# Kernel tuning notes

Hardware: AMD Instinct MI355X
Metric: run time of the kernel (lower is better)

The kernel has to match this reference:

```python
import jax, jax.numpy as jnp
import numpy as np

T, B, I, H, O = 512, 64, 256, 512, 256


def _lstm(x_proj, h0, c0, W_hh, dtype=jnp.float32):
    """Run an LSTM over precomputed input projections.
    x_proj: (T, B, 4H) = x @ W_ih.T + b_ih (+ b_hh folded in).
    PyTorch gate order: i, f, g, o.
    Returns (hs: (T,B,H), h_final: (B,H))."""
    def step(carry, xp_t):
        h, c = carry
        gates = xp_t + h @ W_hh.T  # (B, 4H)
        i, f, g, o = jnp.split(gates, 4, axis=-1)
        c = jax.nn.sigmoid(f) * c + jax.nn.sigmoid(i) * jnp.tanh(g)
        h = jax.nn.sigmoid(o) * jnp.tanh(c)
        return (h, c), h
    (hT, cT), hs = jax.lax.scan(step, (h0, c0), x_proj)
    return hs, hT


def setup_inputs() -> dict:
    key = jax.random.key(0)
    ks = jax.random.split(key, 16)
    s1 = 1.0 / np.sqrt(H)
    u = lambda k, shape: jax.random.uniform(k, shape, jnp.float32, -s1, s1)
    inputs = jax.random.normal(ks[0], (T, B, I), jnp.float32)
    return {
        "inputs": inputs,
        # LSTM1 (input I -> hidden H), PyTorch layout: W_ih (4H, I), W_hh (4H, H)
        "W_ih1": u(ks[1], (4 * H, I)), "W_hh1": u(ks[2], (4 * H, H)),
        "b_ih1": u(ks[3], (4 * H,)), "b_hh1": u(ks[4], (4 * H,)),
        # LSTM2 (hidden H -> hidden H)
        "W_ih2": u(ks[5], (4 * H, H)), "W_hh2": u(ks[6], (4 * H, H)),
        "b_ih2": u(ks[7], (4 * H,)), "b_hh2": u(ks[8], (4 * H,)),
        # Linear H -> O
        "W_lin": u(ks[9], (O, H)), "b_lin": u(ks[10], (O,)),
        # fixed initial hidden/cell states (module buffers in the original)
        "h1_0": jax.random.normal(ks[11], (B, H), jnp.float32),
        "c1_0": jax.random.uniform(ks[12], (B, H), jnp.float32),
        "h2_0": jax.random.normal(ks[13], (B, H), jnp.float32),
        "c2_0": jax.random.normal(ks[14], (B, H), jnp.float32),
    }


def reference(inputs, W_ih1, W_hh1, b_ih1, b_hh1, W_ih2, W_hh2, b_ih2, b_hh2,
              W_lin, b_lin, h1_0, c1_0, h2_0, c2_0):
    # Encoder: precompute input projections for all timesteps at once.
    xp1 = jnp.einsum('tbi,gi->tbg', inputs, W_ih1) + b_ih1 + b_hh1  # (T,B,4H)
    _, h1T = _lstm(xp1, h1_0, c1_0, W_hh1)
    # Decoder input = final encoder hidden repeated T times -> constant projection.
    xp2_one = h1T @ W_ih2.T + b_ih2 + b_hh2  # (B,4H)
    xp2 = jnp.broadcast_to(xp2_one, (T, B, 4 * H))
    out2, _ = _lstm(xp2, h2_0, c2_0, W_hh2)  # (T,B,H)
    out_lin = jnp.einsum('tbh,oh->tbo', out2, W_lin) + b_lin
    return out_lin.reshape(-1, O)  # (T*B, O)
```

## Files before the change

kernel.cpp:

```cpp
#include <hip/hip_runtime.h>
#include <hip/hip_bf16.h>

#define T_ 512
#define B_ 64
#define I_ 256
#define H_ 512
#define O_ 256
#define NGB 32
#define NLB 8
#define NBLK (NGB + NLB)
#define NTHR 512
#define NTOT (NBLK * NTHR)

typedef unsigned short u16;
typedef unsigned int u32;
typedef unsigned long long u64;
typedef short bf16x8 __attribute__((ext_vector_type(8)));
typedef float f32x4 __attribute__((ext_vector_type(4)));
typedef u32 u32x4 __attribute__((ext_vector_type(4)));

#define CT_LIN   0
#define CT_B0    64

#define WS_XBF   4096
#define WS_WHH1  (WS_XBF   + 16777216)
#define WS_WIH1  (WS_WHH1  + 2097152)
#define WS_WIH2  (WS_WIH1  + 1048576)
#define WS_WHH2  (WS_WIH2  + 2097152)
#define WS_WLIN  (WS_WHH2  + 2097152)
#define WS_B1    (WS_WLIN  + 262144)
#define WS_B2    (WS_B1    + 8192)
#define WS_H1T   (WS_B2    + 8192)
#define WS_H2T   (WS_H1T   + 262144)
#define WS_END   (WS_H2T   + 524288)

__device__ __forceinline__ u16 f2bf(float f) {
  union { float f; unsigned u; } v; v.f = f;
  unsigned r = v.u + 0x7FFFu + ((v.u >> 16) & 1u);
  return (u16)(r >> 16);
}
__device__ __forceinline__ float sigm(float x)  { return 1.0f / (1.0f + __expf(-x)); }
__device__ __forceinline__ float tanh_(float x) { return 1.0f - 2.0f / (__expf(2.0f * x) + 1.0f); }
__device__ __forceinline__ bf16x8 ldg8(const u16* p) { return *(const bf16x8*)p; }
__device__ __forceinline__ void ast32(u32* p, u32 v) {
  __hip_atomic_store(p, v, __ATOMIC_RELAXED, __HIP_MEMORY_SCOPE_AGENT);
}
#define MFMA16(a, b, c) __builtin_amdgcn_mfma_f32_16x16x32_bf16((a), (b), (c), 0, 0, 0)

__device__ __forceinline__ void cvt8(const float* s, u16* dst) {
  bf16x8 v;
  #pragma unroll
  for (int jj = 0; jj < 8; jj++) v[jj] = (short)f2bf(s[jj]);
  *(bf16x8*)dst = v;
}

template<bool LINCHK, int SLP>
__device__ __forceinline__ void pollTile(const u32* pbw, u32 tag,
                                         const u32* lfp, int ltgt, u32* pk) {
  while (1) {
    u32 w[16];
    bool ok = true;
    u32x4 A, B2, C2, D2;
    if (LINCHK) {
      u32 lv;
      asm volatile(
        "global_load_dwordx4 %0, %5, off sc0 sc1\n\t"
        "global_load_dwordx4 %1, %5, off offset:16 sc0 sc1\n\t"
        "global_load_dwordx4 %2, %5, off offset:32 sc0 sc1\n\t"
        "global_load_dwordx4 %3, %5, off offset:48 sc0 sc1\n\t"
        "global_load_dword   %4, %6, off sc0 sc1\n\t"
        "s_waitcnt vmcnt(0)"
        : "=&v"(A), "=&v"(B2), "=&v"(C2), "=&v"(D2), "=&v"(lv)
        : "v"(pbw), "v"(lfp)
        : "memory");
      ok = (int)lv >= ltgt;
    } else {
      asm volatile(
        "global_load_dwordx4 %0, %4, off sc0 sc1\n\t"
        "global_load_dwordx4 %1, %4, off offset:16 sc0 sc1\n\t"
        "global_load_dwordx4 %2, %4, off offset:32 sc0 sc1\n\t"
        "global_load_dwordx4 %3, %4, off offset:48 sc0 sc1\n\t"
        "s_waitcnt vmcnt(0)"
        : "=&v"(A), "=&v"(B2), "=&v"(C2), "=&v"(D2)
        : "v"(pbw)
        : "memory");
    }
    #pragma unroll
    for (int m = 0; m < 4; m++) {
      w[m] = A[m]; w[4 + m] = B2[m]; w[8 + m] = C2[m]; w[12 + m] = D2[m];
    }
    #pragma unroll
    for (int m = 0; m < 16; m++) ok = ok && ((w[m] >> 16) == tag);
    if (__all(ok)) {
      #pragma unroll
      for (int m = 0; m < 8; m++)
        pk[m] = (w[2 * m] & 0xFFFFu) | (w[2 * m + 1] << 16);
      return;
    }
    if (SLP) __builtin_amdgcn_s_sleep(SLP);
  }
}

__device__ __forceinline__ void gbar0(u32* cnt, unsigned target) {
  __syncthreads();
  if (threadIdx.x == 0) {
    __threadfence();
    __hip_atomic_fetch_add(cnt, 1u, __ATOMIC_RELAXED, __HIP_MEMORY_SCOPE_AGENT);
    while (__hip_atomic_load(cnt, __ATOMIC_RELAXED, __HIP_MEMORY_SCOPE_AGENT) < target)
      __builtin_amdgcn_s_sleep(2);
    __threadfence();
  }
  __syncthreads();
}

__global__ void init_cnt(char* ws) {
  for (int i = threadIdx.x; i < 1024; i += 256)
    __hip_atomic_store((u32*)ws + i, 0u, __ATOMIC_RELAXED, __HIP_MEMORY_SCOPE_AGENT);
}

__global__ void __launch_bounds__(NTHR, 1) lstm_ae_kernel(
    const float* __restrict__ xin,
    const float* __restrict__ Wih1, const float* __restrict__ Whh1,
    const float* __restrict__ bih1, const float* __restrict__ bhh1,
    const float* __restrict__ Wih2, const float* __restrict__ Whh2,
    const float* __restrict__ bih2, const float* __restrict__ bhh2,
    const float* __restrict__ Wlin, const float* __restrict__ blin,
    const float* __restrict__ h10, const float* __restrict__ c10,
    const float* __restrict__ h20, const float* __restrict__ c20,
    float* __restrict__ out, char* __restrict__ ws) {
  char* ctrl = ws;
  u32* linf  = (u32*)(ctrl + CT_LIN);
  u16* xbf   = (u16*)(ws + WS_XBF);
  u16* whh1f = (u16*)(ws + WS_WHH1);
  u16* wih1f = (u16*)(ws + WS_WIH1);
  u16* wih2f = (u16*)(ws + WS_WIH2);
  u16* whh2f = (u16*)(ws + WS_WHH2);
  u16* wlinf = (u16*)(ws + WS_WLIN);
  float* b1  = (float*)(ws + WS_B1);
  float* b2  = (float*)(ws + WS_B2);
  u32* h1s   = (u32*)(ws + WS_H1T);
  u32* h2s   = (u32*)(ws + WS_H2T);

  __shared__ __align__(16) u16 Ald[16 * 512];
  __shared__ float exch[4 * 16 * 68];

  const int tid = blockIdx.x * NTHR + threadIdx.x;

  for (int c = tid; c < T_ * B_ * I_ / 8; c += NTOT)
    cvt8(xin + c * 8, xbf + c * 8);
  for (int c = tid; c < (1 << 17); c += NTOT) {
    int lane = c & 63, kt = (c >> 6) & 15, g = (c >> 10) & 3, n = c >> 12;
    int row = g * 512 + n * 16 + (lane & 15);
    int k   = kt * 32 + (lane >> 4) * 8;
    cvt8(Whh1 + row * 512 + k, whh1f + c * 8);
  }
  for (int c = tid; c < (1 << 16); c += NTOT) {
    int lane = c & 63, kt = (c >> 6) & 7, g = (c >> 9) & 3, n = c >> 11;
    int row = g * 512 + n * 16 + (lane & 15);
    int k   = kt * 32 + (lane >> 4) * 8;
    cvt8(Wih1 + row * 256 + k, wih1f + c * 8);
  }
  for (int c = tid; c < (1 << 17); c += NTOT) {
    int lane = c & 63, kt = (c >> 6) & 15, g = (c >> 10) & 3, n = c >> 12;
    int row = g * 512 + n * 16 + (lane & 15);
    int k   = kt * 32 + (lane >> 4) * 8;
    cvt8(Wih2 + row * 512 + k, wih2f + c * 8);
    cvt8(Whh2 + row * 512 + k, whh2f + c * 8);
  }
  for (int c = tid; c < (1 << 14); c += NTOT) {
    int lane = c & 63, kt = (c >> 6) & 15, nt = (c >> 10) & 1, l = c >> 11;
    int row = l * 32 + nt * 16 + (lane & 15);
    int k   = kt * 32 + (lane >> 4) * 8;
    cvt8(Wlin + row * 512 + k, wlinf + c * 8);
  }
  for (int i2 = tid; i2 < 2048; i2 += NTOT) {
    b1[i2] = bih1[i2] + bhh1[i2];
    b2[i2] = bih2[i2] + bhh2[i2];
  }
  for (int c = tid; c < (1 << 16); c += NTOT) {
    int slot = c >> 15, rem = c & 32767;
    int mtd = rem >> 13, r2 = rem & 8191, row = r2 >> 9, col = r2 & 511;
    u32 v = 0xFFFF0000u;
    if (slot == 0) v = (u32)f2bf(h10[(mtd * 16 + row) * 512 + col]);
    h1s[c] = v;
  }
  for (int c = tid; c < (1 << 17); c += NTOT) {
    int slot = c >> 15, rem = c & 32767;
    int mtd = rem >> 13, r2 = rem & 8191, row = r2 >> 9, col = r2 & 511;
    u32 v = 0xFFFF0000u;
    if (slot == 0) v = (u32)f2bf(h20[(mtd * 16 + row) * 512 + col]);
    h2s[c] = v;
  }

  gbar0((u32*)(ctrl + CT_B0), NBLK);

  const int lane = threadIdx.x & 63;
  const int w    = threadIdx.x >> 6;
  const int l15  = lane & 15;
  const int l31  = lane & 31;
  const int qd   = lane >> 4;
  const int prow = 2 * w + (lane >> 5);
  const int swz  = (prow & 7) << 4;
  const int pb32 = prow * 512 + l31 * 16;

  #define AFRAG(ktv) (*(const bf16x8*)((const char*)Ald + l15 * 1024 + \
                       (((ktv) * 64 + qd * 16) ^ ((l15 & 7) << 4))))
  #define STAGEA(pk) do { \
      u32x4 v0_ = {(pk)[0], (pk)[1], (pk)[2], (pk)[3]}; \
      u32x4 v1_ = {(pk)[4], (pk)[5], (pk)[6], (pk)[7]}; \
      char* ab_ = (char*)Ald + prow * 1024; \
      *(u32x4*)(ab_ + ((l31 * 32 +  0) ^ swz)) = v0_; \
      *(u32x4*)(ab_ + ((l31 * 32 + 16) ^ swz)) = v1_; \
    } while (0)

  if (blockIdx.x < NGB) {
    const int mt = blockIdx.x >> 3;
    const int j  = blockIdx.x & 7;
    const int g  = w >> 1;
    const int half = w & 1;
    const int nt0 = j * 4 + half * 2;

    bf16x8 Wr0[16], Wr1[16];
    #pragma unroll
    for (int kt = 0; kt < 16; kt++) {
      Wr0[kt] = ldg8(whh1f + ((size_t)((nt0 + 0) * 4 + g) * 16 + kt) * 512 + lane * 8);
      Wr1[kt] = ldg8(whh1f + ((size_t)((nt0 + 1) * 4 + g) * 16 + kt) * 512 + lane * 8);
    }
    const float bg0 = b1[g * 512 + (nt0 + 0) * 16 + l15];
    const float bg1 = b1[g * 512 + (nt0 + 1) * 16 + l15];

    const int hcol = j * 64 + lane;
    float c0v = c10[(mt * 16 + 2 * w + 0) * 512 + hcol];
    float c1v = c10[(mt * 16 + 2 * w + 1) * 512 + hcol];

    const u16* wx0 = wih1f + ((size_t)((nt0 + 0) * 4 + g) * 8) * 512 + lane * 8;
    const u16* wx1 = wih1f + ((size_t)((nt0 + 1) * 4 + g) * 8) * 512 + lane * 8;
    const int axoff = (mt * 16 + l15) * 256 + qd * 8;
    const int sobase = (2 * w) * 512 + j * 64 + lane;

    f32x4 p0, p1;
    {
      p0 = f32x4{bg0, bg0, bg0, bg0};
      p1 = f32x4{bg1, bg1, bg1, bg1};
      const u16* xr = xbf + axoff;
      #pragma unroll
      for (int kt = 0; kt < 8; kt++) {
        bf16x8 ax = ldg8(xr + kt * 32);
        p0 = MFMA16(ax, ldg8(wx0 + kt * 512), p0);
        p1 = MFMA16(ax, ldg8(wx1 + kt * 512), p1);
      }
    }

    for (int t = 0; t < T_; t++) {
      u32 pk[8];
      pollTile<false, 0>(h1s + (size_t)((t & 1) * 4 + mt) * 8192 + pb32,
                         (u32)t, linf, 0, pk);
      STAGEA(pk);
      __syncthreads();
      f32x4 a0 = p0, a1 = p1;
      f32x4 a2 = {0.f, 0.f, 0.f, 0.f}, a3 = {0.f, 0.f, 0.f, 0.f};
      #pragma unroll
      for (int kt = 0; kt < 16; kt += 2) {
        bf16x8 af0 = AFRAG(kt), af1 = AFRAG(kt + 1);
        a0 = MFMA16(af0, Wr0[kt], a0);
        a1 = MFMA16(af0, Wr1[kt], a1);
        a2 = MFMA16(af1, Wr0[kt + 1], a2);
        a3 = MFMA16(af1, Wr1[kt + 1], a3);
      }
      a0 += a2; a1 += a3;
      #pragma unroll
      for (int r = 0; r < 4; r++) {
        exch[g * 1088 + (qd * 4 + r) * 68 + half * 32 +  0 + l15] = a0[r];
        exch[g * 1088 + (qd * 4 + r) * 68 + half * 32 + 16 + l15] = a1[r];
      }
      __syncthreads();
      {
        u32* so = h1s + (size_t)(((t + 1) & 1) * 4 + mt) * 8192 + sobase;
        #pragma unroll
        for (int rr = 0; rr < 2; rr++) {
          int rw = 2 * w + rr;
          float gi = exch[0 * 1088 + rw * 68 + lane];
          float gf = exch[1 * 1088 + rw * 68 + lane];
          float gg = exch[2 * 1088 + rw * 68 + lane];
          float go = exch[3 * 1088 + rw * 68 + lane];
          float cc = rr ? c1v : c0v;
          cc = sigm(gf) * cc + sigm(gi) * tanh_(gg);
          if (rr) c1v = cc; else c0v = cc;
          float hv = sigm(go) * tanh_(cc);
          ast32(so + rr * 512, (u32)f2bf(hv) | ((u32)(t + 1) << 16));
        }
      }
      if (t + 1 < T_) {
        p0 = f32x4{bg0, bg0, bg0, bg0};
        p1 = f32x4{bg1, bg1, bg1, bg1};
        const u16* xr = xbf + (size_t)(t + 1) * (B_ * I_) + axoff;
        #pragma unroll
        for (int kt = 0; kt < 8; kt++) {
          bf16x8 ax = ldg8(xr + kt * 32);
          p0 = MFMA16(ax, ldg8(wx0 + kt * 512), p0);
          p1 = MFMA16(ax, ldg8(wx1 + kt * 512), p1);
        }
      }
    }

    f32x4 q0, q1;
    {
      u32 pk[8];
      pollTile<false, 0>(h1s + (size_t)(0 * 4 + mt) * 8192 + pb32,
                         (u32)T_, linf, 0, pk);
      STAGEA(pk);
      __syncthreads();
      const float b20 = b2[g * 512 + (nt0 + 0) * 16 + l15];
      const float b21 = b2[g * 512 + (nt0 + 1) * 16 + l15];
      q0 = f32x4{b20, b20, b20, b20};
      q1 = f32x4{b21, b21, b21, b21};
      #pragma unroll
      for (int kt = 0; kt < 16; kt++) {
        bf16x8 af = AFRAG(kt);
        q0 = MFMA16(af, ldg8(wih2f + ((size_t)((nt0 + 0) * 4 + g) * 16 + kt) * 512 + lane * 8), q0);
        q1 = MFMA16(af, ldg8(wih2f + ((size_t)((nt0 + 1) * 4 + g) * 16 + kt) * 512 + lane * 8), q1);
      }
      #pragma unroll
      for (int kt = 0; kt < 16; kt++) {
        Wr0[kt] = ldg8(whh2f + ((size_t)((nt0 + 0) * 4 + g) * 16 + kt) * 512 + lane * 8);
        Wr1[kt] = ldg8(whh2f + ((size_t)((nt0 + 1) * 4 + g) * 16 + kt) * 512 + lane * 8);
      }
      c0v = c20[(mt * 16 + 2 * w + 0) * 512 + hcol];
      c1v = c20[(mt * 16 + 2 * w + 1) * 512 + hcol];
      __syncthreads();
    }

    for (int t = 0; t < T_; t++) {
      u32 pk[8];
      const u32* lfp = linf + mt * 2 + (lane & 1);
      const int ltgt = (lane < 2) ? (t - 3) : -1;
      pollTile<true, 0>(h2s + (size_t)((t & 3) * 4 + mt) * 8192 + pb32,
                        (u32)t, lfp, ltgt, pk);
      STAGEA(pk);
      __syncthreads();
      f32x4 a0 = q0, a1 = q1;
      f32x4 a2 = {0.f, 0.f, 0.f, 0.f}, a3 = {0.f, 0.f, 0.f, 0.f};
      #pragma unroll
      for (int kt = 0; kt < 16; kt += 2) {
        bf16x8 af0 = AFRAG(kt), af1 = AFRAG(kt + 1);
        a0 = MFMA16(af0, Wr0[kt], a0);
        a1 = MFMA16(af0, Wr1[kt], a1);
        a2 = MFMA16(af1, Wr0[kt + 1], a2);
        a3 = MFMA16(af1, Wr1[kt + 1], a3);
      }
      a0 += a2; a1 += a3;
      #pragma unroll
      for (int r = 0; r < 4; r++) {
        exch[g * 1088 + (qd * 4 + r) * 68 + half * 32 +  0 + l15] = a0[r];
        exch[g * 1088 + (qd * 4 + r) * 68 + half * 32 + 16 + l15] = a1[r];
      }
      __syncthreads();
      {
        u32* so = h2s + (size_t)(((t + 1) & 3) * 4 + mt) * 8192 + sobase;
        #pragma unroll
        for (int rr = 0; rr < 2; rr++) {
          int rw = 2 * w + rr;
          float gi = exch[0 * 1088 + rw * 68 + lane];
          float gf = exch[1 * 1088 + rw * 68 + lane];
          float gg = exch[2 * 1088 + rw * 68 + lane];
          float go = exch[3 * 1088 + rw * 68 + lane];
          float cc = rr ? c1v : c0v;
          cc = sigm(gf) * cc + sigm(gi) * tanh_(gg);
          if (rr) c1v = cc; else c0v = cc;
          float hv = sigm(go) * tanh_(cc);
          ast32(so + rr * 512, (u32)f2bf(hv) | ((u32)(t + 1) << 16));
        }
      }
    }
  } else {
    const int b  = blockIdx.x - NGB;
    const int mt = b >> 1, qq = b & 1;
    const int to = qq * 8 + w;
    bf16x8 Wl[16];
    #pragma unroll
    for (int kt = 0; kt < 16; kt++)
      Wl[kt] = ldg8(wlinf + ((size_t)to * 16 + kt) * 512 + lane * 8);
    const float bl = blin[to * 16 + l15];
    u32* lfp = linf + mt * 2 + qq;

    for (int s = 0; s < T_; s++) {
      u32 pk[8];
      pollTile<false, 2>(h2s + (size_t)(((s + 1) & 3) * 4 + mt) * 8192 + pb32,
                         (u32)(s + 1), linf, 0, pk);
      STAGEA(pk);
      __syncthreads();
      if (threadIdx.x == 0) ast32(lfp, (u32)(s + 1));
      f32x4 o = {bl, bl, bl, bl};
      #pragma unroll
      for (int kt = 0; kt < 16; kt++) {
        bf16x8 af = AFRAG(kt);
        o = MFMA16(af, Wl[kt], o);
      }
      float* op = out + ((size_t)s * 64 + mt * 16 + qd * 4) * 256 + to * 16 + l15;
      #pragma unroll
      for (int r = 0; r < 4; r++) op[(size_t)r * 256] = o[r];
      __syncthreads();
    }
  }
  #undef AFRAG
  #undef STAGEA
}

extern "C" void kernel_launch(void* const* d_in, const int* in_sizes, int n_in,
                              void* d_out, int out_size, void* d_ws, size_t ws_size,
                              hipStream_t stream) {
  (void)in_sizes; (void)n_in; (void)out_size; (void)ws_size;
  const float* xin  = (const float*)d_in[0];
  const float* Wih1 = (const float*)d_in[1];
  const float* Whh1 = (const float*)d_in[2];
  const float* bih1 = (const float*)d_in[3];
  const float* bhh1 = (const float*)d_in[4];
  const float* Wih2 = (const float*)d_in[5];
  const float* Whh2 = (const float*)d_in[6];
  const float* bih2 = (const float*)d_in[7];
  const float* bhh2 = (const float*)d_in[8];
  const float* Wlin = (const float*)d_in[9];
  const float* blin = (const float*)d_in[10];
  const float* h10  = (const float*)d_in[11];
  const float* c10  = (const float*)d_in[12];
  const float* h20  = (const float*)d_in[13];
  const float* c20  = (const float*)d_in[14];
  float* out = (float*)d_out;
  char* ws   = (char*)d_ws;

  init_cnt<<<dim3(1), dim3(256), 0, stream>>>(ws);

  void* args[] = { (void*)&xin, (void*)&Wih1, (void*)&Whh1, (void*)&bih1, (void*)&bhh1,
                   (void*)&Wih2, (void*)&Whh2, (void*)&bih2, (void*)&bhh2,
                   (void*)&Wlin, (void*)&blin, (void*)&h10, (void*)&c10,
                   (void*)&h20, (void*)&c20, (void*)&out, (void*)&ws };
  hipLaunchCooperativeKernel((void*)lstm_ae_kernel, dim3(NBLK), dim3(NTHR),
                             args, 0, stream);
}
```

Measured before the change: 4.770 ms.

## Reload recurrent weights from L2 each step instead of pinning in registers

The recurrent W_hh fragments are no longer held in registers for the whole sequence. Each timestep now reloads them from global memory (expected to hit L2), with the loads issued before the poll for the previous hidden state so they can overlap the wait. The launch attribute is changed to request two waves per EU, which caps register use. The cost is extra global/L2 traffic on every step of the latency-bound recurrence, and the loads may not fully hide behind the barrier wait.

```diff
diff --git a/kernel.cpp b/kernel.cpp
--- a/kernel.cpp
+++ b/kernel.cpp
@@ -118,7 +118,8 @@
     __hip_atomic_store((u32*)ws + i, 0u, __ATOMIC_RELAXED, __HIP_MEMORY_SCOPE_AGENT);
 }
 
-__global__ void __launch_bounds__(NTHR, 1) lstm_ae_kernel(
+__global__ void __launch_bounds__(NTHR)
+__attribute__((amdgpu_waves_per_eu(2, 2))) lstm_ae_kernel(
     const float* __restrict__ xin,
     const float* __restrict__ Wih1, const float* __restrict__ Whh1,
     const float* __restrict__ bih1, const float* __restrict__ bhh1,
@@ -220,12 +221,11 @@
     const int half = w & 1;
     const int nt0 = j * 4 + half * 2;
 
-    bf16x8 Wr0[16], Wr1[16];
-    #pragma unroll
-    for (int kt = 0; kt < 16; kt++) {
-      Wr0[kt] = ldg8(whh1f + ((size_t)((nt0 + 0) * 4 + g) * 16 + kt) * 512 + lane * 8);
-      Wr1[kt] = ldg8(whh1f + ((size_t)((nt0 + 1) * 4 + g) * 16 + kt) * 512 + lane * 8);
-    }
+    const u16* w1p0 = whh1f + ((size_t)((nt0 + 0) * 4 + g) * 16) * 512 + lane * 8;
+    const u16* w1p1 = whh1f + ((size_t)((nt0 + 1) * 4 + g) * 16) * 512 + lane * 8;
+    const u16* w2p0 = whh2f + ((size_t)((nt0 + 0) * 4 + g) * 16) * 512 + lane * 8;
+    const u16* w2p1 = whh2f + ((size_t)((nt0 + 1) * 4 + g) * 16) * 512 + lane * 8;
+
     const float bg0 = b1[g * 512 + (nt0 + 0) * 16 + l15];
     const float bg1 = b1[g * 512 + (nt0 + 1) * 16 + l15];
 
@@ -252,6 +252,12 @@
     }
 
     for (int t = 0; t < T_; t++) {
+      bf16x8 w0[16], w1[16];
+      #pragma unroll
+      for (int kt = 0; kt < 16; kt++) {
+        w0[kt] = ldg8(w1p0 + kt * 512);
+        w1[kt] = ldg8(w1p1 + kt * 512);
+      }
       u32 pk[8];
       pollTile<false, 0>(h1s + (size_t)((t & 1) * 4 + mt) * 8192 + pb32,
                          (u32)t, linf, 0, pk);
@@ -262,10 +268,10 @@
       #pragma unroll
       for (int kt = 0; kt < 16; kt += 2) {
         bf16x8 af0 = AFRAG(kt), af1 = AFRAG(kt + 1);
-        a0 = MFMA16(af0, Wr0[kt], a0);
-        a1 = MFMA16(af0, Wr1[kt], a1);
-        a2 = MFMA16(af1, Wr0[kt + 1], a2);
-        a3 = MFMA16(af1, Wr1[kt + 1], a3);
+        a0 = MFMA16(af0, w0[kt], a0);
+        a1 = MFMA16(af0, w1[kt], a1);
+        a2 = MFMA16(af1, w0[kt + 1], a2);
+        a3 = MFMA16(af1, w1[kt + 1], a3);
       }
       a0 += a2; a1 += a3;
       #pragma unroll
@@ -320,17 +326,18 @@
         q0 = MFMA16(af, ldg8(wih2f + ((size_t)((nt0 + 0) * 4 + g) * 16 + kt) * 512 + lane * 8), q0);
         q1 = MFMA16(af, ldg8(wih2f + ((size_t)((nt0 + 1) * 4 + g) * 16 + kt) * 512 + lane * 8), q1);
       }
-      #pragma unroll
-      for (int kt = 0; kt < 16; kt++) {
-        Wr0[kt] = ldg8(whh2f + ((size_t)((nt0 + 0) * 4 + g) * 16 + kt) * 512 + lane * 8);
-        Wr1[kt] = ldg8(whh2f + ((size_t)((nt0 + 1) * 4 + g) * 16 + kt) * 512 + lane * 8);
-      }
       c0v = c20[(mt * 16 + 2 * w + 0) * 512 + hcol];
       c1v = c20[(mt * 16 + 2 * w + 1) * 512 + hcol];
       __syncthreads();
     }
 
     for (int t = 0; t < T_; t++) {
+      bf16x8 w0[16], w1[16];
+      #pragma unroll
+      for (int kt = 0; kt < 16; kt++) {
+        w0[kt] = ldg8(w2p0 + kt * 512);
+        w1[kt] = ldg8(w2p1 + kt * 512);
+      }
       u32 pk[8];
       const u32* lfp = linf + mt * 2 + (lane & 1);
       const int ltgt = (lane < 2) ? (t - 3) : -1;
@@ -343,10 +350,10 @@
       #pragma unroll
       for (int kt = 0; kt < 16; kt += 2) {
         bf16x8 af0 = AFRAG(kt), af1 = AFRAG(kt + 1);
-        a0 = MFMA16(af0, Wr0[kt], a0);
-        a1 = MFMA16(af0, Wr1[kt], a1);
-        a2 = MFMA16(af1, Wr0[kt + 1], a2);
-        a3 = MFMA16(af1, Wr1[kt + 1], a3);
+        a0 = MFMA16(af0, w0[kt], a0);
+        a1 = MFMA16(af0, w1[kt], a1);
+        a2 = MFMA16(af1, w0[kt + 1], a2);
+        a3 = MFMA16(af1, w1[kt + 1], a3);
       }
       a0 += a2; a1 += a3;
       #pragma unroll
```

After: 6.969 ms. 46.1% more time.
